# Optimization experiments

Measured on AMD Instinct MI355X. Metric: run time of the kernel, lower is better.

Reference implementation:

```python
import jax, jax.numpy as jnp
import numpy as np

N = 50000          # nodes
E = 1600000        # edges
F_IN = 128         # node_features
H = 256            # hidden_dim
A = 16             # action_dim
G = 64             # num graphs in batch


def _sage_conv(x, src, dst, Wl, bl, Wr, num_nodes):
    # PyG SAGEConv (aggr='mean'): out = lin_l(mean_{j in N(i)} x_j) + lin_r(x_i)
    msgs = x[src]                                              # [E, F] gather
    agg = jax.ops.segment_sum(msgs, dst, num_segments=num_nodes)
    cnt = jax.ops.segment_sum(jnp.ones((src.shape[0], 1), x.dtype), dst,
                              num_segments=num_nodes)
    mean = agg / jnp.maximum(cnt, 1.0)                         # [N, F]
    return mean @ Wl + bl + x @ Wr


def setup_inputs() -> dict:
    key = jax.random.key(0)
    ks = jax.random.split(key, 16)
    s = lambda k, sh: jax.random.normal(k, sh, dtype=jnp.float32) * (1.0 / np.sqrt(sh[0]))
    inp = {
        "x": jax.random.normal(ks[0], (N, F_IN), dtype=jnp.float32),
        "edge_index": jax.random.randint(ks[1], (2, E), 0, N, dtype=jnp.int32),
        "batch": jnp.sort(jax.random.randint(ks[2], (N,), 0, G, dtype=jnp.int32)),
        # SAGEConv 1
        "Wl1": s(ks[3], (F_IN, H)), "bl1": jnp.zeros((H,), jnp.float32), "Wr1": s(ks[4], (F_IN, H)),
        # SAGEConv 2
        "Wl2": s(ks[5], (H, H)), "bl2": jnp.zeros((H,), jnp.float32), "Wr2": s(ks[6], (H, H)),
        # actor MLP
        "Wa1": s(ks[7], (H, H)), "ba1": jnp.zeros((H,), jnp.float32),
        "Wa2": s(ks[8], (H, A)), "ba2": jnp.zeros((A,), jnp.float32),
        # critic MLP
        "Wc1": s(ks[9], (H, H)), "bc1": jnp.zeros((H,), jnp.float32),
        "Wc2": s(ks[10], (H, 1)), "bc2": jnp.zeros((1,), jnp.float32),
    }
    return inp


def reference(x, edge_index, batch, Wl1, bl1, Wr1, Wl2, bl2, Wr2,
              Wa1, ba1, Wa2, ba2, Wc1, bc1, Wc2, bc2):
    src, dst = edge_index[0], edge_index[1]
    h = jax.nn.relu(_sage_conv(x, src, dst, Wl1, bl1, Wr1, N))
    h = jax.nn.relu(_sage_conv(h, src, dst, Wl2, bl2, Wr2, N))
    # global_mean_pool over graph ids
    pooled = jax.ops.segment_sum(h, batch, num_segments=G)
    gcnt = jax.ops.segment_sum(jnp.ones((N, 1), h.dtype), batch, num_segments=G)
    g = pooled / jnp.maximum(gcnt, 1.0)                        # [G, H]
    mu = jax.nn.relu(g @ Wa1 + ba1) @ Wa2 + ba2                # [G, A]
    value = jax.nn.relu(g @ Wc1 + bc1) @ Wc2 + bc2             # [G, 1]
    return mu, value
```

## Files before the change

### kernel.cpp

```cpp
#include <hip/hip_runtime.h>
#include <hip/hip_bf16.h>
#include <hip/hip_fp8.h>

#define NN 50000
#define NE 1600000
#define FIN 128
#define HH 256
#define GG 64
#define AA 16
#define NRANGE 4
#define RSZ (NN / NRANGE)
#define CAP 128

typedef __attribute__((ext_vector_type(8))) short short8;
typedef __attribute__((ext_vector_type(4))) float f32x4;
typedef __attribute__((ext_vector_type(4))) int   i32x4;
typedef __attribute__((ext_vector_type(4))) uint  u32x4;

static __device__ __forceinline__ ushort f2b(float f) {
    union { __hip_bfloat16 h; ushort u; } v; v.h = __float2bfloat16(f); return v.u;
}
static __device__ __forceinline__ float b2f_lo(uint a) {
    union { float f; uint u; } v; v.u = a << 16; return v.f;
}
template<int SEL>
static __device__ __forceinline__ float f8tof(uint u) {
#if __has_builtin(__builtin_amdgcn_cvt_f32_fp8)
    return __builtin_amdgcn_cvt_f32_fp8(u, SEL);
#else
    union { unsigned char c; __hip_fp8_e4m3 f; } v;
    v.c = (u >> (SEL * 8)) & 0xFF;
    return (float)v.f;
#endif
}
static __device__ __forceinline__ unsigned char ftof8(float f) {
    __hip_fp8_e4m3 v(f);
    return *reinterpret_cast<unsigned char*>(&v);
}

__global__ void k_prep(const float* __restrict__ x, ushort* __restrict__ xb,
                       unsigned char* __restrict__ xf8,
                       const float* __restrict__ Wl1, const float* __restrict__ Wr1,
                       ushort* __restrict__ Wt1,
                       const float* __restrict__ Wl2, const float* __restrict__ Wr2,
                       ushort* __restrict__ Wt2,
                       int* __restrict__ cnt, float* __restrict__ gpool) {
    int b = blockIdx.x, t = threadIdx.x;
    if (b < 6250) {
        int i = b * 256 + t;
        float4 v = reinterpret_cast<const float4*>(x)[i];
        ushort4 o; o.x = f2b(v.x); o.y = f2b(v.y); o.z = f2b(v.z); o.w = f2b(v.w);
        reinterpret_cast<ushort4*>(xb)[i] = o;
        uchar4 p; p.x = ftof8(v.x); p.y = ftof8(v.y); p.z = ftof8(v.z); p.w = ftof8(v.w);
        reinterpret_cast<uchar4*>(xf8)[i] = p;
    } else if (b < 6506) {
        int i = (b - 6250) * 256 + t;
        int n = i / 256, k = i % 256;
        float v = (k < 128) ? Wl1[k * HH + n] : Wr1[(k - 128) * HH + n];
        Wt1[i] = f2b(v);
    } else if (b < 7018) {
        int i = (b - 6506) * 256 + t;
        int n = i / 512, k = i % 512;
        float v = (k < 256) ? Wl2[k * HH + n] : Wr2[(k - 256) * HH + n];
        Wt2[i] = f2b(v);
    } else if (b < 7214) {
        int i = (b - 7018) * 256 + t;
        if (i < NN) cnt[i] = 0;
    } else {
        int i = (b - 7214) * 256 + t;
        gpool[i] = 0.0f;
    }
}

__global__ void k_fill(const int* __restrict__ src, const int* __restrict__ dst,
                       int* __restrict__ cnt, ushort* __restrict__ csr16) {
    int range = blockIdx.x & (NRANGE - 1);
    int i = (blockIdx.x / NRANGE) * 256 + threadIdx.x;
    if (i >= NE / 4) return;
    i32x4 d = __builtin_nontemporal_load(reinterpret_cast<const i32x4*>(dst) + i);
    i32x4 s = __builtin_nontemporal_load(reinterpret_cast<const i32x4*>(src) + i);
    int lo = range * RSZ, hi = lo + RSZ;
    if (d.x >= lo && d.x < hi) {
        int sl = atomicAdd(&cnt[d.x], 1);
        if (sl < CAP) csr16[(size_t)d.x * CAP + sl] = (ushort)s.x;
    }
    if (d.y >= lo && d.y < hi) {
        int sl = atomicAdd(&cnt[d.y], 1);
        if (sl < CAP) csr16[(size_t)d.y * CAP + sl] = (ushort)s.y;
    }
    if (d.z >= lo && d.z < hi) {
        int sl = atomicAdd(&cnt[d.z], 1);
        if (sl < CAP) csr16[(size_t)d.z * CAP + sl] = (ushort)s.z;
    }
    if (d.w >= lo && d.w < hi) {
        int sl = atomicAdd(&cnt[d.w], 1);
        if (sl < CAP) csr16[(size_t)d.w * CAP + sl] = (ushort)s.w;
    }
}

template<int C>
__global__ void __launch_bounds__(256) k_gatherf8(
        const int* __restrict__ cnt, const ushort* __restrict__ csr16,
        const unsigned char* __restrict__ feat, ushort* __restrict__ agg) {
    constexpr int V = C / 64;
    int wid = threadIdx.x >> 6, lane = threadIdx.x & 63;
    int node = blockIdx.x * 4 + wid;
    if (node >= NN) return;
    int deg = cnt[node]; if (deg > CAP) deg = CAP;
    const ushort* row = csr16 + (size_t)node * CAP;
    const unsigned char* fp = feat + lane * V;
    float acc[V];
#pragma unroll
    for (int i = 0; i < V; i++) acc[i] = 0.0f;

    int t = 0;
    for (; t + 3 < deg; t += 4) {
        int s0 = __builtin_nontemporal_load(row + t);
        int s1 = __builtin_nontemporal_load(row + t + 1);
        int s2 = __builtin_nontemporal_load(row + t + 2);
        int s3 = __builtin_nontemporal_load(row + t + 3);
        if constexpr (V == 2) {
            uint u0 = *(const ushort*)(fp + (size_t)s0 * C);
            uint u1 = *(const ushort*)(fp + (size_t)s1 * C);
            uint u2 = *(const ushort*)(fp + (size_t)s2 * C);
            uint u3 = *(const ushort*)(fp + (size_t)s3 * C);
            acc[0] += (f8tof<0>(u0) + f8tof<0>(u1)) + (f8tof<0>(u2) + f8tof<0>(u3));
            acc[1] += (f8tof<1>(u0) + f8tof<1>(u1)) + (f8tof<1>(u2) + f8tof<1>(u3));
        } else {
            uint u0 = *(const uint*)(fp + (size_t)s0 * C);
            uint u1 = *(const uint*)(fp + (size_t)s1 * C);
            uint u2 = *(const uint*)(fp + (size_t)s2 * C);
            uint u3 = *(const uint*)(fp + (size_t)s3 * C);
            acc[0] += (f8tof<0>(u0) + f8tof<0>(u1)) + (f8tof<0>(u2) + f8tof<0>(u3));
            acc[1] += (f8tof<1>(u0) + f8tof<1>(u1)) + (f8tof<1>(u2) + f8tof<1>(u3));
            acc[2] += (f8tof<2>(u0) + f8tof<2>(u1)) + (f8tof<2>(u2) + f8tof<2>(u3));
            acc[3] += (f8tof<3>(u0) + f8tof<3>(u1)) + (f8tof<3>(u2) + f8tof<3>(u3));
        }
    }
    for (; t < deg; ++t) {
        int s0 = __builtin_nontemporal_load(row + t);
        if constexpr (V == 2) {
            uint u0 = *(const ushort*)(fp + (size_t)s0 * C);
            acc[0] += f8tof<0>(u0); acc[1] += f8tof<1>(u0);
        } else {
            uint u0 = *(const uint*)(fp + (size_t)s0 * C);
            acc[0] += f8tof<0>(u0); acc[1] += f8tof<1>(u0);
            acc[2] += f8tof<2>(u0); acc[3] += f8tof<3>(u0);
        }
    }

    float r = __builtin_amdgcn_rcpf(deg > 1 ? (float)deg : 1.0f);
    if constexpr (V == 2) {
        uint o = (uint)f2b(acc[0] * r) | ((uint)f2b(acc[1] * r) << 16);
        *(uint*)(agg + (size_t)node * C + lane * 2) = o;
    } else {
        uint2 o;
        o.x = (uint)f2b(acc[0] * r) | ((uint)f2b(acc[1] * r) << 16);
        o.y = (uint)f2b(acc[2] * r) | ((uint)f2b(acc[3] * r) << 16);
        *(uint2*)(agg + (size_t)node * C + lane * 4) = o;
    }
}

template<int K>
__global__ void __launch_bounds__(256) k_sage_mfma(
        const ushort* __restrict__ agg, const ushort* __restrict__ xin,
        const ushort* __restrict__ Wt, const float* __restrict__ bias,
        ushort* __restrict__ outb, unsigned char* __restrict__ out8) {
    constexpr int KH = K / 2;
    constexpr int LDP = 40;
    __shared__ ushort As[128 * LDP];
    __shared__ ushort Bs[256 * LDP];

    const int tid  = threadIdx.x;
    const int lane = tid & 63;
    const int w    = tid >> 6;
    const int base = blockIdx.x * 128;
    const int r    = lane & 15;
    const int kh   = lane >> 4;
    const int wcol = w * 64;

    f32x4 acc[8][4];
#pragma unroll
    for (int m = 0; m < 8; m++)
#pragma unroll
        for (int n = 0; n < 4; n++) acc[m][n] = (f32x4){0.f, 0.f, 0.f, 0.f};

    const int frowA = tid >> 1;
    const int fqA   = tid & 1;
    const int frowB = tid >> 2;
    const int fqB   = tid & 3;
    int fnode = base + frowA; if (fnode >= NN) fnode = 0;

    for (int k0 = 0; k0 < K; k0 += 32) {
        __syncthreads();
        {
            const ushort* srcp = (k0 < KH)
                ? agg + (size_t)fnode * KH + k0 + fqA * 16
                : xin + (size_t)fnode * KH + (k0 - KH) + fqA * 16;
            u32x4 a0 = *(const u32x4*)srcp;
            u32x4 a1 = *(const u32x4*)(srcp + 8);
            *(u32x4*)(&As[frowA * LDP + fqA * 16])     = a0;
            *(u32x4*)(&As[frowA * LDP + fqA * 16 + 8]) = a1;
        }
#pragma unroll
        for (int s = 0; s < 4; s++) {
            int c = frowB + s * 64;
            *(u32x4*)(&Bs[c * LDP + fqB * 8]) =
                *(const u32x4*)(Wt + (size_t)c * K + k0 + fqB * 8);
        }
        __syncthreads();

        short8 av[8], bv[4];
#pragma unroll
        for (int m = 0; m < 8; m++)
            av[m] = *(const short8*)(&As[(m * 16 + r) * LDP + kh * 8]);
#pragma unroll
        for (int n = 0; n < 4; n++)
            bv[n] = *(const short8*)(&Bs[(wcol + n * 16 + r) * LDP + kh * 8]);
#pragma unroll
        for (int m = 0; m < 8; m++)
#pragma unroll
            for (int n = 0; n < 4; n++)
                acc[m][n] = __builtin_amdgcn_mfma_f32_16x16x32_bf16(
                    av[m], bv[n], acc[m][n], 0, 0, 0);
    }

    float bj[4];
#pragma unroll
    for (int n = 0; n < 4; n++) bj[n] = bias[wcol + n * 16 + r];

#pragma unroll
    for (int m = 0; m < 8; m++) {
        int rowbase = base + m * 16 + (lane >> 4) * 4;
#pragma unroll
        for (int reg = 0; reg < 4; reg++) {
            int nd = rowbase + reg;
            if (nd < NN) {
#pragma unroll
                for (int n = 0; n < 4; n++) {
                    float v = acc[m][n][reg] + bj[n];
                    v = v > 0.0f ? v : 0.0f;
                    outb[(size_t)nd * HH + wcol + n * 16 + r] = f2b(v);
                    if (out8) out8[(size_t)nd * HH + wcol + n * 16 + r] = ftof8(v);
                }
            }
        }
    }
}

__global__ void k_pool(const ushort* __restrict__ h, const int* __restrict__ batch,
                       float* __restrict__ gpool) {
    __shared__ int sb[32];
    int j = threadIdx.x;
    int base = blockIdx.x * 32;
    int n = NN - base; if (n > 32) n = 32;
    if (j < n) sb[j] = batch[base + j];
    __syncthreads();
    float acc = 0.0f;
    int cur = sb[0];
    for (int t = 0; t < n; t++) {
        int g = sb[t];
        if (g != cur) {
            atomicAdd(&gpool[cur * HH + j], acc);
            acc = 0.0f;
            cur = g;
        }
        acc += b2f_lo((uint)h[(size_t)(base + t) * HH + j]);
    }
    atomicAdd(&gpool[cur * HH + j], acc);
}

__global__ void k_head(const float* __restrict__ gpool, const int* __restrict__ batch,
                       const float* __restrict__ Wa1, const float* __restrict__ ba1,
                       const float* __restrict__ Wa2, const float* __restrict__ ba2,
                       const float* __restrict__ Wc1, const float* __restrict__ bc1,
                       const float* __restrict__ Wc2, const float* __restrict__ bc2,
                       float* __restrict__ outp) {
    __shared__ float gv[HH], ha[HH], hc[HH];
    __shared__ float cs;
    int g = blockIdx.x, j = threadIdx.x;
    if (j == 0) {
        int lo = 0, hi = NN;
        while (lo < hi) { int m = (lo + hi) >> 1; if (batch[m] < g) lo = m + 1; else hi = m; }
        int a = lo; lo = 0; hi = NN;
        while (lo < hi) { int m = (lo + hi) >> 1; if (batch[m] < g + 1) lo = m + 1; else hi = m; }
        cs = (float)(lo - a);
    }
    __syncthreads();
    float c = cs > 1.0f ? cs : 1.0f;
    gv[j] = gpool[g * HH + j] / c;
    __syncthreads();
    float a_acc = ba1[j], c_acc = bc1[j];
#pragma unroll 2
    for (int k = 0; k < HH; k += 4) {
        float4 g4 = *reinterpret_cast<const float4*>(&gv[k]);
        const float* WA = Wa1 + k * HH + j;
        const float* WC = Wc1 + k * HH + j;
        a_acc += g4.x * WA[0] + g4.y * WA[HH] + g4.z * WA[2 * HH] + g4.w * WA[3 * HH];
        c_acc += g4.x * WC[0] + g4.y * WC[HH] + g4.z * WC[2 * HH] + g4.w * WC[3 * HH];
    }
    ha[j] = a_acc > 0.0f ? a_acc : 0.0f;
    hc[j] = c_acc > 0.0f ? c_acc : 0.0f;
    __syncthreads();
    if (j < AA) {
        float m = ba2[j];
        for (int k = 0; k < HH; k++) m += ha[k] * Wa2[k * AA + j];
        outp[g * AA + j] = m;
    } else if (j == AA) {
        float v = bc2[0];
        for (int k = 0; k < HH; k++) v += hc[k] * Wc2[k];
        outp[GG * AA + g] = v;
    }
}

extern "C" void kernel_launch(void* const* d_in, const int* in_sizes, int n_in,
                              void* d_out, int out_size, void* d_ws, size_t ws_size,
                              hipStream_t stream) {
    const float* x     = (const float*)d_in[0];
    const int*   ei    = (const int*)d_in[1];
    const int*   batch = (const int*)d_in[2];
    const float* Wl1 = (const float*)d_in[3];
    const float* bl1 = (const float*)d_in[4];
    const float* Wr1 = (const float*)d_in[5];
    const float* Wl2 = (const float*)d_in[6];
    const float* bl2 = (const float*)d_in[7];
    const float* Wr2 = (const float*)d_in[8];
    const float* Wa1 = (const float*)d_in[9];
    const float* ba1 = (const float*)d_in[10];
    const float* Wa2 = (const float*)d_in[11];
    const float* ba2 = (const float*)d_in[12];
    const float* Wc1 = (const float*)d_in[13];
    const float* bc1 = (const float*)d_in[14];
    const float* Wc2 = (const float*)d_in[15];
    const float* bc2 = (const float*)d_in[16];
    float* out = (float*)d_out;

    const int* srcv = ei;
    const int* dstv = ei + NE;

    char* ws = (char*)d_ws;
    int*    cnt      = (int*)(ws + 0);
    float*  gpool    = (float*)(ws + 200192);
    ushort* csr16    = (ushort*)(ws + 265728);
    ushort* xb       = (ushort*)(ws + 13065728);
    ushort* agg1b    = (ushort*)(ws + 25865728);
    ushort* h1b      = (ushort*)(ws + 38665728);
    ushort* agg2b    = (ushort*)(ws + 64265728);
    ushort* Wt1      = (ushort*)(ws + 89865728);
    ushort* Wt2      = (ushort*)(ws + 89996800);
    unsigned char* xf8  = (unsigned char*)(ws + 90258944);
    unsigned char* h1f8 = (unsigned char*)(ws + 96658944);

    k_prep<<<7278, 256, 0, stream>>>(x, xb, xf8, Wl1, Wr1, Wt1, Wl2, Wr2, Wt2,
                                     cnt, gpool);

    const int nch = (NE / 4 + 255) / 256;
    k_fill<<<nch * NRANGE, 256, 0, stream>>>(srcv, dstv, cnt, csr16);

    k_gatherf8<FIN><<<(NN + 3) / 4, 256, 0, stream>>>(cnt, csr16, xf8, agg1b);
    k_sage_mfma<2 * FIN><<<(NN + 127) / 128, 256, 0, stream>>>(agg1b, xb, Wt1, bl1, h1b, h1f8);

    k_gatherf8<HH><<<(NN + 3) / 4, 256, 0, stream>>>(cnt, csr16, h1f8, agg2b);
    k_sage_mfma<2 * HH><<<(NN + 127) / 128, 256, 0, stream>>>(agg2b, h1b, Wt2, bl2, agg2b, nullptr);

    k_pool<<<(NN + 31) / 32, 256, 0, stream>>>(agg2b, batch, gpool);
    k_head<<<GG, 256, 0, stream>>>(gpool, batch, Wa1, ba1, Wa2, ba2, Wc1, bc1,
                                   Wc2, bc2, out);
}
```

Before: 357.3 us.

## Replace range-partitioned CSR fill with 8-way privatized per-bucket adjacency lists

The edge-bucketing kernel no longer rescans all edges four times by destination range. Each block now writes into one of 8 private count/adjacency copies, chosen by block index, with 24 slots per node per copy. The gather kernel walks all 8 sub-lists per node and sums their degrees. This removes redundant edge reads and spreads atomic contention, but the gather now does 8 count loads and shorter, branchier inner loops per node. It also uses a larger workspace and a larger zeroing pass, and a node can drop edges if one copy receives more than 24 of them.

```diff
diff --git a/kernel.cpp b/kernel.cpp
--- a/kernel.cpp
+++ b/kernel.cpp
@@ -8,9 +8,8 @@
 #define HH 256
 #define GG 64
 #define AA 16
-#define NRANGE 4
-#define RSZ (NN / NRANGE)
-#define CAP 128
+#define NW 8
+#define WCAP 24
 
 typedef __attribute__((ext_vector_type(8))) short short8;
 typedef __attribute__((ext_vector_type(4))) float f32x4;
@@ -44,7 +43,7 @@
                        ushort* __restrict__ Wt1,
                        const float* __restrict__ Wl2, const float* __restrict__ Wr2,
                        ushort* __restrict__ Wt2,
-                       int* __restrict__ cnt, float* __restrict__ gpool) {
+                       int* __restrict__ cntw, float* __restrict__ gpool) {
     int b = blockIdx.x, t = threadIdx.x;
     if (b < 6250) {
         int i = b * 256 + t;
@@ -63,89 +62,79 @@
         int n = i / 512, k = i % 512;
         float v = (k < 256) ? Wl2[k * HH + n] : Wr2[(k - 256) * HH + n];
         Wt2[i] = f2b(v);
-    } else if (b < 7214) {
+    } else if (b < 8581) {
         int i = (b - 7018) * 256 + t;
-        if (i < NN) cnt[i] = 0;
+        if (i < NW * NN) cntw[i] = 0;
     } else {
-        int i = (b - 7214) * 256 + t;
+        int i = (b - 8581) * 256 + t;
         gpool[i] = 0.0f;
     }
 }
 
 __global__ void k_fill(const int* __restrict__ src, const int* __restrict__ dst,
-                       int* __restrict__ cnt, ushort* __restrict__ csr16) {
-    int range = blockIdx.x & (NRANGE - 1);
-    int i = (blockIdx.x / NRANGE) * 256 + threadIdx.x;
+                       int* __restrict__ cntw, ushort* __restrict__ csr16) {
+    const int w = blockIdx.x & (NW - 1);
+    const int i = blockIdx.x * 256 + threadIdx.x;
     if (i >= NE / 4) return;
     i32x4 d = __builtin_nontemporal_load(reinterpret_cast<const i32x4*>(dst) + i);
     i32x4 s = __builtin_nontemporal_load(reinterpret_cast<const i32x4*>(src) + i);
-    int lo = range * RSZ, hi = lo + RSZ;
-    if (d.x >= lo && d.x < hi) {
-        int sl = atomicAdd(&cnt[d.x], 1);
-        if (sl < CAP) csr16[(size_t)d.x * CAP + sl] = (ushort)s.x;
-    }
-    if (d.y >= lo && d.y < hi) {
-        int sl = atomicAdd(&cnt[d.y], 1);
-        if (sl < CAP) csr16[(size_t)d.y * CAP + sl] = (ushort)s.y;
-    }
-    if (d.z >= lo && d.z < hi) {
-        int sl = atomicAdd(&cnt[d.z], 1);
-        if (sl < CAP) csr16[(size_t)d.z * CAP + sl] = (ushort)s.z;
-    }
-    if (d.w >= lo && d.w < hi) {
-        int sl = atomicAdd(&cnt[d.w], 1);
-        if (sl < CAP) csr16[(size_t)d.w * CAP + sl] = (ushort)s.w;
+    int* cw = cntw + (size_t)w * NN;
+    ushort* rw = csr16 + (size_t)w * NN * WCAP;
+    int dv[4] = {d.x, d.y, d.z, d.w};
+    int sv[4] = {s.x, s.y, s.z, s.w};
+#pragma unroll
+    for (int k = 0; k < 4; k++) {
+        int sl = atomicAdd(&cw[dv[k]], 1);
+        if (sl < WCAP) rw[(size_t)dv[k] * WCAP + sl] = (ushort)sv[k];
     }
 }
 
 template<int C>
 __global__ void __launch_bounds__(256) k_gatherf8(
-        const int* __restrict__ cnt, const ushort* __restrict__ csr16,
+        const int* __restrict__ cntw, const ushort* __restrict__ csr16,
         const unsigned char* __restrict__ feat, ushort* __restrict__ agg) {
     constexpr int V = C / 64;
     int wid = threadIdx.x >> 6, lane = threadIdx.x & 63;
     int node = blockIdx.x * 4 + wid;
     if (node >= NN) return;
-    int deg = cnt[node]; if (deg > CAP) deg = CAP;
-    const ushort* row = csr16 + (size_t)node * CAP;
     const unsigned char* fp = feat + lane * V;
     float acc[V];
 #pragma unroll
     for (int i = 0; i < V; i++) acc[i] = 0.0f;
 
-    int t = 0;
-    for (; t + 3 < deg; t += 4) {
-        int s0 = __builtin_nontemporal_load(row + t);
-        int s1 = __builtin_nontemporal_load(row + t + 1);
-        int s2 = __builtin_nontemporal_load(row + t + 2);
-        int s3 = __builtin_nontemporal_load(row + t + 3);
-        if constexpr (V == 2) {
-            uint u0 = *(const ushort*)(fp + (size_t)s0 * C);
-            uint u1 = *(const ushort*)(fp + (size_t)s1 * C);
-            uint u2 = *(const ushort*)(fp + (size_t)s2 * C);
-            uint u3 = *(const ushort*)(fp + (size_t)s3 * C);
-            acc[0] += (f8tof<0>(u0) + f8tof<0>(u1)) + (f8tof<0>(u2) + f8tof<0>(u3));
-            acc[1] += (f8tof<1>(u0) + f8tof<1>(u1)) + (f8tof<1>(u2) + f8tof<1>(u3));
-        } else {
-            uint u0 = *(const uint*)(fp + (size_t)s0 * C);
-            uint u1 = *(const uint*)(fp + (size_t)s1 * C);
-            uint u2 = *(const uint*)(fp + (size_t)s2 * C);
-            uint u3 = *(const uint*)(fp + (size_t)s3 * C);
-            acc[0] += (f8tof<0>(u0) + f8tof<0>(u1)) + (f8tof<0>(u2) + f8tof<0>(u3));
-            acc[1] += (f8tof<1>(u0) + f8tof<1>(u1)) + (f8tof<1>(u2) + f8tof<1>(u3));
-            acc[2] += (f8tof<2>(u0) + f8tof<2>(u1)) + (f8tof<2>(u2) + f8tof<2>(u3));
-            acc[3] += (f8tof<3>(u0) + f8tof<3>(u1)) + (f8tof<3>(u2) + f8tof<3>(u3));
-        }
-    }
-    for (; t < deg; ++t) {
-        int s0 = __builtin_nontemporal_load(row + t);
-        if constexpr (V == 2) {
-            uint u0 = *(const ushort*)(fp + (size_t)s0 * C);
-            acc[0] += f8tof<0>(u0); acc[1] += f8tof<1>(u0);
-        } else {
-            uint u0 = *(const uint*)(fp + (size_t)s0 * C);
-            acc[0] += f8tof<0>(u0); acc[1] += f8tof<1>(u0);
-            acc[2] += f8tof<2>(u0); acc[3] += f8tof<3>(u0);
+    int deg = 0;
+#pragma unroll
+    for (int w = 0; w < NW; w++) {
+        int dw = cntw[(size_t)w * NN + node]; if (dw > WCAP) dw = WCAP;
+        deg += dw;
+        const ushort* row = csr16 + ((size_t)w * NN + node) * WCAP;
+        int t = 0;
+        for (; t + 1 < dw; t += 2) {
+            int s0 = row[t], s1 = row[t + 1];
+            if constexpr (V == 2) {
+                uint u0 = *(const ushort*)(fp + (size_t)s0 * C);
+                uint u1 = *(const ushort*)(fp + (size_t)s1 * C);
+                acc[0] += f8tof<0>(u0) + f8tof<0>(u1);
+                acc[1] += f8tof<1>(u0) + f8tof<1>(u1);
+            } else {
+                uint u0 = *(const uint*)(fp + (size_t)s0 * C);
+                uint u1 = *(const uint*)(fp + (size_t)s1 * C);
+                acc[0] += f8tof<0>(u0) + f8tof<0>(u1);
+                acc[1] += f8tof<1>(u0) + f8tof<1>(u1);
+                acc[2] += f8tof<2>(u0) + f8tof<2>(u1);
+                acc[3] += f8tof<3>(u0) + f8tof<3>(u1);
+            }
+        }
+        if (t < dw) {
+            int s0 = row[t];
+            if constexpr (V == 2) {
+                uint u0 = *(const ushort*)(fp + (size_t)s0 * C);
+                acc[0] += f8tof<0>(u0); acc[1] += f8tof<1>(u0);
+            } else {
+                uint u0 = *(const uint*)(fp + (size_t)s0 * C);
+                acc[0] += f8tof<0>(u0); acc[1] += f8tof<1>(u0);
+                acc[2] += f8tof<2>(u0); acc[3] += f8tof<3>(u0);
+            }
         }
     }
 
@@ -339,28 +328,27 @@
     const int* dstv = ei + NE;
 
     char* ws = (char*)d_ws;
-    int*    cnt      = (int*)(ws + 0);
-    float*  gpool    = (float*)(ws + 200192);
-    ushort* csr16    = (ushort*)(ws + 265728);
-    ushort* xb       = (ushort*)(ws + 13065728);
-    ushort* agg1b    = (ushort*)(ws + 25865728);
-    ushort* h1b      = (ushort*)(ws + 38665728);
-    ushort* agg2b    = (ushort*)(ws + 64265728);
-    ushort* Wt1      = (ushort*)(ws + 89865728);
-    ushort* Wt2      = (ushort*)(ws + 89996800);
-    unsigned char* xf8  = (unsigned char*)(ws + 90258944);
-    unsigned char* h1f8 = (unsigned char*)(ws + 96658944);
-
-    k_prep<<<7278, 256, 0, stream>>>(x, xb, xf8, Wl1, Wr1, Wt1, Wl2, Wr2, Wt2,
-                                     cnt, gpool);
-
-    const int nch = (NE / 4 + 255) / 256;
-    k_fill<<<nch * NRANGE, 256, 0, stream>>>(srcv, dstv, cnt, csr16);
-
-    k_gatherf8<FIN><<<(NN + 3) / 4, 256, 0, stream>>>(cnt, csr16, xf8, agg1b);
+    int*    cntw     = (int*)(ws + 0);
+    float*  gpool    = (float*)(ws + 1600000);
+    ushort* csr16    = (ushort*)(ws + 1665536);
+    ushort* xb       = (ushort*)(ws + 20865536);
+    ushort* agg1b    = (ushort*)(ws + 33665536);
+    ushort* h1b      = (ushort*)(ws + 46465536);
+    ushort* agg2b    = (ushort*)(ws + 72065536);
+    ushort* Wt1      = (ushort*)(ws + 97665536);
+    ushort* Wt2      = (ushort*)(ws + 97796608);
+    unsigned char* xf8  = (unsigned char*)(ws + 98058752);
+    unsigned char* h1f8 = (unsigned char*)(ws + 104458752);
+
+    k_prep<<<8645, 256, 0, stream>>>(x, xb, xf8, Wl1, Wr1, Wt1, Wl2, Wr2, Wt2,
+                                     cntw, gpool);
+
+    k_fill<<<(NE / 4 + 255) / 256, 256, 0, stream>>>(srcv, dstv, cntw, csr16);
+
+    k_gatherf8<FIN><<<(NN + 3) / 4, 256, 0, stream>>>(cntw, csr16, xf8, agg1b);
     k_sage_mfma<2 * FIN><<<(NN + 127) / 128, 256, 0, stream>>>(agg1b, xb, Wt1, bl1, h1b, h1f8);
 
-    k_gatherf8<HH><<<(NN + 3) / 4, 256, 0, stream>>>(cnt, csr16, h1f8, agg2b);
+    k_gatherf8<HH><<<(NN + 3) / 4, 256, 0, stream>>>(cntw, csr16, h1f8, agg2b);
     k_sage_mfma<2 * HH><<<(NN + 127) / 128, 256, 0, stream>>>(agg2b, h1b, Wt2, bl2, agg2b, nullptr);
 
     k_pool<<<(NN + 31) / 32, 256, 0, stream>>>(agg2b, batch, gpool);
```

Result: slower. 452.2 us (+26.6%).
